# Kernel tuning notes

Hardware: AMD Instinct MI355X
Metric: run time of the kernel (lower is better)

The kernel has to match this reference:

```python
import jax, jax.numpy as jnp
import numpy as np

D = 1024      # feat_dim
H = 16        # n_heads
HD = D // H   # head_dim
G = 32        # number of image/text groups
P = 128       # patch tokens per image
T = 32        # text tokens per caption
SUM_P = G * P # 4096
BT = G * T    # 1024


def setup_inputs() -> dict:
    key = jax.random.key(0)
    ks = jax.random.split(key, 16)
    s = (6.0 / (2 * D)) ** 0.5  # xavier_uniform bound
    def xavier(k):
        return jax.random.uniform(k, (D, D), jnp.float32, -s, s)
    return {
        "V_token": jax.random.normal(ks[0], (SUM_P, D), jnp.float32),
        "L_token": jax.random.normal(ks[1], (BT, D), jnp.float32),
        "image_split_list": jnp.full((G,), P, dtype=jnp.int32),
        "text_split_list": jnp.full((G,), T, dtype=jnp.int32),
        "Wq_w": xavier(ks[2]), "Wq_b": jnp.zeros((D,), jnp.float32),
        "Wk_w": xavier(ks[3]), "Wk_b": jnp.zeros((D,), jnp.float32),
        "Wv_w": xavier(ks[4]), "Wv_b": jnp.zeros((D,), jnp.float32),
        "Wo_w": xavier(ks[5]), "Wo_b": jnp.zeros((D,), jnp.float32),
        "Wm_w": xavier(ks[6]), "Wm_b": jnp.zeros((D,), jnp.float32),
        "Wv2_w": xavier(ks[7]), "Wv2_b": jnp.zeros((D,), jnp.float32),
    }


def reference(V_token, L_token, image_split_list, text_split_list,
              Wq_w, Wq_b, Wk_w, Wk_b, Wv_w, Wv_b,
              Wo_w, Wo_b, Wm_w, Wm_b, Wv2_w, Wv2_b):
    sum_p, bt = V_token.shape[0], L_token.shape[0]
    g = image_split_list.shape[0]
    # segment ids (equivalent to torch.cat of torch.full per group)
    v_seg = jnp.repeat(jnp.arange(g), image_split_list, total_repeat_length=sum_p)
    l_seg = jnp.repeat(jnp.arange(g), text_split_list, total_repeat_length=bt)
    mask = v_seg[:, None] != l_seg[None, :]  # [sum_p, bt], True = masked out

    Q = (V_token @ Wq_w.T + Wq_b).reshape(sum_p, H, HD)
    K = (L_token @ Wk_w.T + Wk_b).reshape(bt, H, HD)
    Vl = (L_token @ Wv_w.T + Wv_b).reshape(bt, H, HD)

    scores = jnp.einsum('phd,thd->hpt', Q, K) / (HD ** 0.5)  # [H, sum_p, bt]
    scores = jnp.where(mask[None, :, :], -jnp.inf, scores)
    attn = jax.nn.softmax(scores, axis=-1)
    ctx = jnp.einsum('hpt,thd->phd', attn, Vl).reshape(sum_p, D)

    out = ctx @ Wo_w.T + Wo_b
    mu = out @ Wm_w.T + Wm_b
    log_var = out @ Wv2_w.T + Wv2_b
    return mu, log_var, attn
```

## Files before the change

### kernel.cpp

```cpp
#include <hip/hip_runtime.h>
#include <hip/hip_fp16.h>

typedef _Float16 f16x8 __attribute__((ext_vector_type(8)));
typedef _Float16 f16x4 __attribute__((ext_vector_type(4)));
typedef float f32x4_t __attribute__((ext_vector_type(4)));

struct CvtArgs {
  const float* src[8];
  _Float16* dst[8];
  int n4[8];
};

__global__ __launch_bounds__(256) void cvt_all(CvtArgs a) {
  const int t = blockIdx.y;
  const float4* __restrict__ in = (const float4*)a.src[t];
  f16x4* __restrict__ out = (f16x4*)a.dst[t];
  const int n4 = a.n4[t];
  const int stride = gridDim.x * blockDim.x;
  for (int i = blockIdx.x * blockDim.x + threadIdx.x; i < n4; i += stride) {
    float4 v = in[i];
    f16x4 h;
    h[0] = (_Float16)v.x; h[1] = (_Float16)v.y; h[2] = (_Float16)v.z; h[3] = (_Float16)v.w;
    out[i] = h;
  }
}

template <bool OUTH>
__device__ __forceinline__ void gemm_tile(const _Float16* __restrict__ A,
                                          const _Float16* __restrict__ W,
                                          const float* __restrict__ bias,
                                          void* __restrict__ Cv, int tm, int tn) {
  __shared__ _Float16 Ash[128][40];
  __shared__ _Float16 Bsh[64][40];

  const int tid = threadIdx.x;
  const int lane = tid & 63;
  const int wave = tid >> 6;
  const int wr = wave >> 1;
  const int wc = wave & 1;

  const int ar = tid >> 1;
  const int ac = (tid & 1) * 16;
  const int br = tid >> 2;
  const int bc = (tid & 3) * 8;

  const _Float16* Ag = A + (size_t)(tm + ar) * 1024 + ac;
  const _Float16* Bg = W + (size_t)(tn + br) * 1024 + bc;

  f32x4_t acc[4][2];
#pragma unroll
  for (int m = 0; m < 4; ++m)
#pragma unroll
    for (int n = 0; n < 2; ++n) acc[m][n] = (f32x4_t){0.f, 0.f, 0.f, 0.f};

  uint4 pa0 = *(const uint4*)(Ag);
  uint4 pa1 = *(const uint4*)(Ag + 8);
  uint4 pb = *(const uint4*)(Bg);

  const int fr = lane & 15;
  const int kc = (lane >> 4) * 8;

#pragma unroll 1
  for (int kt = 0; kt < 32; ++kt) {
    __syncthreads();
    *(uint4*)&Ash[ar][ac] = pa0;
    *(uint4*)&Ash[ar][ac + 8] = pa1;
    *(uint4*)&Bsh[br][bc] = pb;
    __syncthreads();
    if (kt + 1 < 32) {
      const int ko = (kt + 1) * 32;
      pa0 = *(const uint4*)(Ag + ko);
      pa1 = *(const uint4*)(Ag + ko + 8);
      pb = *(const uint4*)(Bg + ko);
    }
    f16x8 af[4], bf[2];
#pragma unroll
    for (int m = 0; m < 4; ++m) af[m] = *(const f16x8*)&Ash[wr * 64 + m * 16 + fr][kc];
#pragma unroll
    for (int n = 0; n < 2; ++n) bf[n] = *(const f16x8*)&Bsh[wc * 32 + n * 16 + fr][kc];
#pragma unroll
    for (int m = 0; m < 4; ++m)
#pragma unroll
      for (int n = 0; n < 2; ++n)
        acc[m][n] = __builtin_amdgcn_mfma_f32_16x16x32_f16(af[m], bf[n], acc[m][n], 0, 0, 0);
  }

  const int cr = (lane >> 4) * 4;
  const int cc = lane & 15;
#pragma unroll
  for (int m = 0; m < 4; ++m) {
#pragma unroll
    for (int n = 0; n < 2; ++n) {
      const int col = tn + wc * 32 + n * 16 + cc;
      const float bv = bias[col];
#pragma unroll
      for (int r = 0; r < 4; ++r) {
        const int row = tm + wr * 64 + m * 16 + cr + r;
        float v = acc[m][n][r] + bv;
        if (OUTH)
          ((_Float16*)Cv)[(size_t)row * 1024 + col] = (_Float16)v;
        else
          ((float*)Cv)[(size_t)row * 1024 + col] = v;
      }
    }
  }
}

__global__ __launch_bounds__(256) void gemm_qkv_fill(
    const _Float16* __restrict__ hV, const _Float16* __restrict__ hL,
    const _Float16* __restrict__ hWq, const _Float16* __restrict__ hWk,
    const _Float16* __restrict__ hWv,
    const float* __restrict__ bq, const float* __restrict__ bk, const float* __restrict__ bv,
    float* __restrict__ Qf, float* __restrict__ Kf, float* __restrict__ Vf,
    float* __restrict__ attn) {
  const int z = blockIdx.z;
  if (z == 3) {
    const int bl = blockIdx.y * 32 + blockIdx.x;
    float4* base = (float4*)attn + (size_t)bl * 16384;
    const float4 z4 = {0.f, 0.f, 0.f, 0.f};
#pragma unroll
    for (int c = threadIdx.x; c < 16384; c += 256) base[c] = z4;
    return;
  }
  if (z != 0 && blockIdx.x >= 8) return;

  const _Float16* A = (z == 0) ? hV : hL;
  const _Float16* W = (z == 0) ? hWq : (z == 1) ? hWk : hWv;
  const float* bias = (z == 0) ? bq : (z == 1) ? bk : bv;
  float* C = (z == 0) ? Qf : (z == 1) ? Kf : Vf;
  gemm_tile<false>(A, W, bias, (void*)C, blockIdx.x * 128, blockIdx.y * 64);
}

__global__ __launch_bounds__(256) void gemm_wo(
    const _Float16* __restrict__ ctx, const _Float16* __restrict__ hWo,
    const float* __restrict__ bo, _Float16* __restrict__ outh) {
  gemm_tile<true>(ctx, hWo, bo, (void*)outh, blockIdx.x * 128, blockIdx.y * 64);
}

__global__ __launch_bounds__(256) void gemm_mv_fill(
    const _Float16* __restrict__ outh,
    const _Float16* __restrict__ hWm, const _Float16* __restrict__ hWv2,
    const float* __restrict__ bm, const float* __restrict__ bv2,
    float* __restrict__ mu, float* __restrict__ logv, float* __restrict__ attn) {
  const int z = blockIdx.z;
  if (z == 2) {
    const int bl = blockIdx.y * 32 + blockIdx.x;
    const int wave = threadIdx.x >> 6;
    const int lane = threadIdx.x & 63;
    const float4 z4 = {0.f, 0.f, 0.f, 0.f};
#pragma unroll
    for (int i = 0; i < 16; ++i) {
      const int rowIdx = bl * 64 + i * 4 + wave;
      const int p = rowIdx & 4095;
      const int g8 = (p >> 7) * 8;
      float4* row = (float4*)(attn + ((size_t)(8 + (rowIdx >> 12)) * 4096 + p) * 1024);
#pragma unroll
      for (int c = lane; c < 256; c += 64) {
        if (c < g8 || c >= g8 + 8) row[c] = z4;
      }
    }
    return;
  }
  const _Float16* W = z ? hWv2 : hWm;
  const float* bias = z ? bv2 : bm;
  float* C = z ? logv : mu;
  gemm_tile<false>(outh, W, bias, (void*)C, blockIdx.x * 128, blockIdx.y * 64);
}

__global__ __launch_bounds__(256) void attn_kernel(
    const float* __restrict__ Q, const float* __restrict__ Kf, const float* __restrict__ Vf,
    float* __restrict__ attn_out,
    _Float16* __restrict__ ctx) {
  const int g = blockIdx.x;
  const int h = blockIdx.y;

  __shared__ float Ksh[32][68];
  __shared__ float Vsh[32][68];
  __shared__ float Arow[128][33];

  const int tid = threadIdx.x;

#pragma unroll
  for (int i = 0; i < 8; ++i) {
    int idx = tid + i * 256;
    int t = idx >> 6, d = idx & 63;
    Ksh[t][d] = Kf[(size_t)(g * 32 + t) * 1024 + h * 64 + d];
    Vsh[t][d] = Vf[(size_t)(g * 32 + t) * 1024 + h * 64 + d];
  }
  __syncthreads();

  const int p = tid >> 1;
  const int half = tid & 1;

  float4 qv[16];
  const float* qrow = Q + (size_t)(g * 128 + p) * 1024 + h * 64;
#pragma unroll
  for (int i = 0; i < 16; ++i) qv[i] = ((const float4*)qrow)[i];

  float s[16];
#pragma unroll
  for (int j = 0; j < 16; ++j) {
    int t = half * 16 + j;
    float acc = 0.f;
#pragma unroll
    for (int d4 = 0; d4 < 16; ++d4) {
      float4 kv = *(const float4*)&Ksh[t][d4 * 4];
      acc += qv[d4].x * kv.x + qv[d4].y * kv.y + qv[d4].z * kv.z + qv[d4].w * kv.w;
    }
    s[j] = acc * 0.125f;
  }

  float m = s[0];
#pragma unroll
  for (int j = 1; j < 16; ++j) m = fmaxf(m, s[j]);
  m = fmaxf(m, __shfl_xor(m, 1));
  float e[16];
  float sum = 0.f;
#pragma unroll
  for (int j = 0; j < 16; ++j) {
    e[j] = __expf(s[j] - m);
    sum += e[j];
  }
  sum += __shfl_xor(sum, 1);
  const float inv = 1.0f / sum;

  float* arow_out =
      attn_out + (size_t)h * 4096 * 1024 + (size_t)(g * 128 + p) * 1024 + g * 32 + half * 16;
#pragma unroll
  for (int j = 0; j < 16; ++j) {
    float a = e[j] * inv;
    arow_out[j] = a;
    Arow[p][half * 16 + j] = a;
  }
  __syncthreads();

  float4 acc4[8];
#pragma unroll
  for (int i = 0; i < 8; ++i) acc4[i] = (float4){0.f, 0.f, 0.f, 0.f};
#pragma unroll
  for (int t = 0; t < 32; ++t) {
    float av = Arow[p][t];
#pragma unroll
    for (int d4 = 0; d4 < 8; ++d4) {
      float4 v = *(const float4*)&Vsh[t][half * 32 + d4 * 4];
      acc4[d4].x += av * v.x;
      acc4[d4].y += av * v.y;
      acc4[d4].z += av * v.z;
      acc4[d4].w += av * v.w;
    }
  }
  _Float16* crow = ctx + (size_t)(g * 128 + p) * 1024 + h * 64 + half * 32;
#pragma unroll
  for (int i = 0; i < 4; ++i) {
    f16x8 hv;
    float4 lo = acc4[i * 2], hi = acc4[i * 2 + 1];
    hv[0] = (_Float16)lo.x; hv[1] = (_Float16)lo.y;
    hv[2] = (_Float16)lo.z; hv[3] = (_Float16)lo.w;
    hv[4] = (_Float16)hi.x; hv[5] = (_Float16)hi.y;
    hv[6] = (_Float16)hi.z; hv[7] = (_Float16)hi.w;
    *(f16x8*)&crow[i * 8] = hv;
  }
}

extern "C" void kernel_launch(void* const* d_in, const int* in_sizes, int n_in,
                              void* d_out, int out_size, void* d_ws, size_t ws_size,
                              hipStream_t stream) {
  const float* V_token = (const float*)d_in[0];
  const float* L_token = (const float*)d_in[1];
  const float* Wq_w = (const float*)d_in[4];
  const float* Wq_b = (const float*)d_in[5];
  const float* Wk_w = (const float*)d_in[6];
  const float* Wk_b = (const float*)d_in[7];
  const float* Wv_w = (const float*)d_in[8];
  const float* Wv_b = (const float*)d_in[9];
  const float* Wo_w = (const float*)d_in[10];
  const float* Wo_b = (const float*)d_in[11];
  const float* Wm_w = (const float*)d_in[12];
  const float* Wm_b = (const float*)d_in[13];
  const float* Wv2_w = (const float*)d_in[14];
  const float* Wv2_b = (const float*)d_in[15];

  char* ws = (char*)d_ws;
  _Float16* hV = (_Float16*)ws;   ws += (size_t)4096 * 1024 * 2;
  _Float16* hL = (_Float16*)ws;   ws += (size_t)1024 * 1024 * 2;
  _Float16* hWq = (_Float16*)ws;  ws += (size_t)1024 * 1024 * 2;
  _Float16* hWk = (_Float16*)ws;  ws += (size_t)1024 * 1024 * 2;
  _Float16* hWv = (_Float16*)ws;  ws += (size_t)1024 * 1024 * 2;
  _Float16* hWo = (_Float16*)ws;  ws += (size_t)1024 * 1024 * 2;
  _Float16* hWm = (_Float16*)ws;  ws += (size_t)1024 * 1024 * 2;
  _Float16* hWv2 = (_Float16*)ws; ws += (size_t)1024 * 1024 * 2;
  float* Qf = (float*)ws;         ws += (size_t)4096 * 1024 * 4;
  float* Kf = (float*)ws;         ws += (size_t)1024 * 1024 * 4;
  float* Vf = (float*)ws;         ws += (size_t)1024 * 1024 * 4;
  _Float16* ctx = (_Float16*)ws;  ws += (size_t)4096 * 1024 * 2;
  _Float16* outh = (_Float16*)ws; ws += (size_t)4096 * 1024 * 2;

  float* mu = (float*)d_out;
  float* logv = mu + (size_t)4096 * 1024;
  float* attn = mu + (size_t)2 * 4096 * 1024;

  CvtArgs ca;
  ca.src[0] = V_token; ca.dst[0] = hV;  ca.n4[0] = 4096 * 1024 / 4;
  ca.src[1] = L_token; ca.dst[1] = hL;  ca.n4[1] = 1024 * 1024 / 4;
  ca.src[2] = Wq_w;  ca.dst[2] = hWq;  ca.n4[2] = 1024 * 1024 / 4;
  ca.src[3] = Wk_w;  ca.dst[3] = hWk;  ca.n4[3] = 1024 * 1024 / 4;
  ca.src[4] = Wv_w;  ca.dst[4] = hWv;  ca.n4[4] = 1024 * 1024 / 4;
  ca.src[5] = Wo_w;  ca.dst[5] = hWo;  ca.n4[5] = 1024 * 1024 / 4;
  ca.src[6] = Wm_w;  ca.dst[6] = hWm;  ca.n4[6] = 1024 * 1024 / 4;
  ca.src[7] = Wv2_w; ca.dst[7] = hWv2; ca.n4[7] = 1024 * 1024 / 4;
  hipLaunchKernelGGL(cvt_all, dim3(128, 8), dim3(256), 0, stream, ca);

  hipLaunchKernelGGL(gemm_qkv_fill, dim3(32, 16, 4), dim3(256), 0, stream,
                     hV, hL, hWq, hWk, hWv, Wq_b, Wk_b, Wv_b, Qf, Kf, Vf, attn);

  hipLaunchKernelGGL(attn_kernel, dim3(32, 16), dim3(256), 0, stream, Qf, Kf, Vf, attn, ctx);

  hipLaunchKernelGGL(gemm_wo, dim3(32, 16), dim3(256), 0, stream, ctx, hWo, Wo_b, outh);

  hipLaunchKernelGGL(gemm_mv_fill, dim3(32, 16, 3), dim3(256), 0, stream,
                     outh, hWm, hWv2, Wm_b, Wv2_b, mu, logv, attn);
}
```

Measured before the change: 175.5 us.

## Double-buffer GEMM tiles with BK=64, store Q/K/V in fp16, flatten grids

The GEMM tile now uses double-buffered shared memory with a K-step of 64, which halves the barriers per K iteration and overlaps global prefetch with MFMA work. Q, K and V are written as fp16 instead of fp32, which cuts intermediate traffic; the attention kernel converts them back to float. The grids are flattened to 1D, which removes idle blocks for the K/V projections and gives the zero-fill blocks larger chunks. Q/K/V storage loses precision, and the larger shared tiles may reduce occupancy.

```diff
diff --git a/kernel.cpp b/kernel.cpp
--- a/kernel.cpp
+++ b/kernel.cpp
@@ -26,12 +26,12 @@
 }
 
 template <bool OUTH>
-__device__ __forceinline__ void gemm_tile(const _Float16* __restrict__ A,
-                                          const _Float16* __restrict__ W,
-                                          const float* __restrict__ bias,
-                                          void* __restrict__ Cv, int tm, int tn) {
-  __shared__ _Float16 Ash[128][40];
-  __shared__ _Float16 Bsh[64][40];
+__device__ __forceinline__ void gemm_tile64(const _Float16* __restrict__ A,
+                                            const _Float16* __restrict__ W,
+                                            const float* __restrict__ bias,
+                                            void* __restrict__ Cv, int tm, int tn) {
+  __shared__ _Float16 Ash[2][128][72];
+  __shared__ _Float16 Bsh[2][64][72];
 
   const int tid = threadIdx.x;
   const int lane = tid & 63;
@@ -39,13 +39,10 @@
   const int wr = wave >> 1;
   const int wc = wave & 1;
 
-  const int ar = tid >> 1;
-  const int ac = (tid & 1) * 16;
-  const int br = tid >> 2;
-  const int bc = (tid & 3) * 8;
-
-  const _Float16* Ag = A + (size_t)(tm + ar) * 1024 + ac;
-  const _Float16* Bg = W + (size_t)(tn + br) * 1024 + bc;
+  const int srow = tid >> 3;
+  const int scol = (tid & 7) * 8;
+  const _Float16* Ag = A + (size_t)(tm + srow) * 1024 + scol;
+  const _Float16* Bg = W + (size_t)(tn + srow) * 1024 + scol;
 
   f32x4_t acc[4][2];
 #pragma unroll
@@ -53,36 +50,61 @@
 #pragma unroll
     for (int n = 0; n < 2; ++n) acc[m][n] = (f32x4_t){0.f, 0.f, 0.f, 0.f};
 
-  uint4 pa0 = *(const uint4*)(Ag);
-  uint4 pa1 = *(const uint4*)(Ag + 8);
-  uint4 pb = *(const uint4*)(Bg);
+  uint4 ra[4], rb[2];
+
+#pragma unroll
+  for (int i = 0; i < 4; ++i) ra[i] = *(const uint4*)(Ag + (size_t)(i * 32) * 1024);
+#pragma unroll
+  for (int i = 0; i < 2; ++i) rb[i] = *(const uint4*)(Bg + (size_t)(i * 32) * 1024);
+#pragma unroll
+  for (int i = 0; i < 4; ++i) *(uint4*)&Ash[0][srow + i * 32][scol] = ra[i];
+#pragma unroll
+  for (int i = 0; i < 2; ++i) *(uint4*)&Bsh[0][srow + i * 32][scol] = rb[i];
+#pragma unroll
+  for (int i = 0; i < 4; ++i) ra[i] = *(const uint4*)(Ag + (size_t)(i * 32) * 1024 + 64);
+#pragma unroll
+  for (int i = 0; i < 2; ++i) rb[i] = *(const uint4*)(Bg + (size_t)(i * 32) * 1024 + 64);
+  __syncthreads();
 
   const int fr = lane & 15;
   const int kc = (lane >> 4) * 8;
 
 #pragma unroll 1
-  for (int kt = 0; kt < 32; ++kt) {
+  for (int t = 0; t < 16; ++t) {
+    const int cur = t & 1;
+    f16x8 af[2][4], bf[2][2];
+#pragma unroll
+    for (int ks = 0; ks < 2; ++ks) {
+#pragma unroll
+      for (int m = 0; m < 4; ++m)
+        af[ks][m] = *(const f16x8*)&Ash[cur][wr * 64 + m * 16 + fr][ks * 32 + kc];
+#pragma unroll
+      for (int n = 0; n < 2; ++n)
+        bf[ks][n] = *(const f16x8*)&Bsh[cur][wc * 32 + n * 16 + fr][ks * 32 + kc];
+    }
+#pragma unroll
+    for (int ks = 0; ks < 2; ++ks)
+#pragma unroll
+      for (int m = 0; m < 4; ++m)
+#pragma unroll
+        for (int n = 0; n < 2; ++n)
+          acc[m][n] =
+              __builtin_amdgcn_mfma_f32_16x16x32_f16(af[ks][m], bf[ks][n], acc[m][n], 0, 0, 0);
+    if (t < 15) {
+#pragma unroll
+      for (int i = 0; i < 4; ++i) *(uint4*)&Ash[cur ^ 1][srow + i * 32][scol] = ra[i];
+#pragma unroll
+      for (int i = 0; i < 2; ++i) *(uint4*)&Bsh[cur ^ 1][srow + i * 32][scol] = rb[i];
+    }
+    if (t < 14) {
+#pragma unroll
+      for (int i = 0; i < 4; ++i)
+        ra[i] = *(const uint4*)(Ag + (size_t)(i * 32) * 1024 + (t + 2) * 64);
+#pragma unroll
+      for (int i = 0; i < 2; ++i)
+        rb[i] = *(const uint4*)(Bg + (size_t)(i * 32) * 1024 + (t + 2) * 64);
+    }
     __syncthreads();
-    *(uint4*)&Ash[ar][ac] = pa0;
-    *(uint4*)&Ash[ar][ac + 8] = pa1;
-    *(uint4*)&Bsh[br][bc] = pb;
-    __syncthreads();
-    if (kt + 1 < 32) {
-      const int ko = (kt + 1) * 32;
-      pa0 = *(const uint4*)(Ag + ko);
-      pa1 = *(const uint4*)(Ag + ko + 8);
-      pb = *(const uint4*)(Bg + ko);
-    }
-    f16x8 af[4], bf[2];
-#pragma unroll
-    for (int m = 0; m < 4; ++m) af[m] = *(const f16x8*)&Ash[wr * 64 + m * 16 + fr][kc];
-#pragma unroll
-    for (int n = 0; n < 2; ++n) bf[n] = *(const f16x8*)&Bsh[wc * 32 + n * 16 + fr][kc];
-#pragma unroll
-    for (int m = 0; m < 4; ++m)
-#pragma unroll
-      for (int n = 0; n < 2; ++n)
-        acc[m][n] = __builtin_amdgcn_mfma_f32_16x16x32_f16(af[m], bf[n], acc[m][n], 0, 0, 0);
   }
 
   const int cr = (lane >> 4) * 4;
@@ -111,30 +133,34 @@
     const _Float16* __restrict__ hWq, const _Float16* __restrict__ hWk,
     const _Float16* __restrict__ hWv,
     const float* __restrict__ bq, const float* __restrict__ bk, const float* __restrict__ bv,
-    float* __restrict__ Qf, float* __restrict__ Kf, float* __restrict__ Vf,
+    _Float16* __restrict__ Qh, _Float16* __restrict__ Kh, _Float16* __restrict__ Vh,
     float* __restrict__ attn) {
-  const int z = blockIdx.z;
-  if (z == 3) {
-    const int bl = blockIdx.y * 32 + blockIdx.x;
-    float4* base = (float4*)attn + (size_t)bl * 16384;
+  int b = blockIdx.x;
+  if (b < 256) {
+    float4* base = (float4*)attn + (size_t)b * 32768;
     const float4 z4 = {0.f, 0.f, 0.f, 0.f};
-#pragma unroll
-    for (int c = threadIdx.x; c < 16384; c += 256) base[c] = z4;
-    return;
-  }
-  if (z != 0 && blockIdx.x >= 8) return;
-
-  const _Float16* A = (z == 0) ? hV : hL;
-  const _Float16* W = (z == 0) ? hWq : (z == 1) ? hWk : hWv;
-  const float* bias = (z == 0) ? bq : (z == 1) ? bk : bv;
-  float* C = (z == 0) ? Qf : (z == 1) ? Kf : Vf;
-  gemm_tile<false>(A, W, bias, (void*)C, blockIdx.x * 128, blockIdx.y * 64);
+    for (int i = threadIdx.x; i < 32768; i += 256) base[i] = z4;
+    return;
+  }
+  b -= 256;
+  if (b < 512) {
+    gemm_tile64<true>(hV, hWq, bq, (void*)Qh, (b >> 4) * 128, (b & 15) * 64);
+    return;
+  }
+  b -= 512;
+  if (b < 128) {
+    gemm_tile64<true>(hL, hWk, bk, (void*)Kh, (b >> 4) * 128, (b & 15) * 64);
+    return;
+  }
+  b -= 128;
+  gemm_tile64<true>(hL, hWv, bv, (void*)Vh, (b >> 4) * 128, (b & 15) * 64);
 }
 
 __global__ __launch_bounds__(256) void gemm_wo(
     const _Float16* __restrict__ ctx, const _Float16* __restrict__ hWo,
     const float* __restrict__ bo, _Float16* __restrict__ outh) {
-  gemm_tile<true>(ctx, hWo, bo, (void*)outh, blockIdx.x * 128, blockIdx.y * 64);
+  const int b = blockIdx.x;
+  gemm_tile64<true>(ctx, hWo, bo, (void*)outh, (b >> 4) * 128, (b & 15) * 64);
 }
 
 __global__ __launch_bounds__(256) void gemm_mv_fill(
@@ -142,33 +168,33 @@
     const _Float16* __restrict__ hWm, const _Float16* __restrict__ hWv2,
     const float* __restrict__ bm, const float* __restrict__ bv2,
     float* __restrict__ mu, float* __restrict__ logv, float* __restrict__ attn) {
-  const int z = blockIdx.z;
-  if (z == 2) {
-    const int bl = blockIdx.y * 32 + blockIdx.x;
+  int b = blockIdx.x;
+  if (b < 256) {
     const int wave = threadIdx.x >> 6;
     const int lane = threadIdx.x & 63;
     const float4 z4 = {0.f, 0.f, 0.f, 0.f};
-#pragma unroll
-    for (int i = 0; i < 16; ++i) {
-      const int rowIdx = bl * 64 + i * 4 + wave;
+    for (int i = 0; i < 32; ++i) {
+      const int rowIdx = b * 128 + i * 4 + wave;
       const int p = rowIdx & 4095;
       const int g8 = (p >> 7) * 8;
       float4* row = (float4*)(attn + ((size_t)(8 + (rowIdx >> 12)) * 4096 + p) * 1024);
-#pragma unroll
-      for (int c = lane; c < 256; c += 64) {
+      for (int c = lane; c < 256; c += 64)
         if (c < g8 || c >= g8 + 8) row[c] = z4;
-      }
-    }
-    return;
-  }
-  const _Float16* W = z ? hWv2 : hWm;
-  const float* bias = z ? bv2 : bm;
-  float* C = z ? logv : mu;
-  gemm_tile<false>(outh, W, bias, (void*)C, blockIdx.x * 128, blockIdx.y * 64);
+    }
+    return;
+  }
+  b -= 256;
+  if (b < 512) {
+    gemm_tile64<false>(outh, hWm, bm, (void*)mu, (b >> 4) * 128, (b & 15) * 64);
+    return;
+  }
+  b -= 512;
+  gemm_tile64<false>(outh, hWv2, bv2, (void*)logv, (b >> 4) * 128, (b & 15) * 64);
 }
 
 __global__ __launch_bounds__(256) void attn_kernel(
-    const float* __restrict__ Q, const float* __restrict__ Kf, const float* __restrict__ Vf,
+    const _Float16* __restrict__ Qh, const _Float16* __restrict__ Kh,
+    const _Float16* __restrict__ Vh,
     float* __restrict__ attn_out,
     _Float16* __restrict__ ctx) {
   const int g = blockIdx.x;
@@ -179,34 +205,37 @@
   __shared__ float Arow[128][33];
 
   const int tid = threadIdx.x;
-
-#pragma unroll
-  for (int i = 0; i < 8; ++i) {
-    int idx = tid + i * 256;
-    int t = idx >> 6, d = idx & 63;
-    Ksh[t][d] = Kf[(size_t)(g * 32 + t) * 1024 + h * 64 + d];
-    Vsh[t][d] = Vf[(size_t)(g * 32 + t) * 1024 + h * 64 + d];
+  {
+    const int r = tid >> 3, c8 = (tid & 7) * 8;
+    f16x8 kv = *(const f16x8*)(Kh + (size_t)(g * 32 + r) * 1024 + h * 64 + c8);
+    f16x8 vv = *(const f16x8*)(Vh + (size_t)(g * 32 + r) * 1024 + h * 64 + c8);
+#pragma unroll
+    for (int j = 0; j < 8; ++j) {
+      Ksh[r][c8 + j] = (float)kv[j];
+      Vsh[r][c8 + j] = (float)vv[j];
+    }
   }
   __syncthreads();
 
   const int p = tid >> 1;
   const int half = tid & 1;
 
-  float4 qv[16];
-  const float* qrow = Q + (size_t)(g * 128 + p) * 1024 + h * 64;
-#pragma unroll
-  for (int i = 0; i < 16; ++i) qv[i] = ((const float4*)qrow)[i];
+  float qf[64];
+  const f16x8* qp = (const f16x8*)(Qh + (size_t)(g * 128 + p) * 1024 + h * 64);
+#pragma unroll
+  for (int i = 0; i < 8; ++i) {
+    f16x8 v = qp[i];
+#pragma unroll
+    for (int j = 0; j < 8; ++j) qf[i * 8 + j] = (float)v[j];
+  }
 
   float s[16];
 #pragma unroll
   for (int j = 0; j < 16; ++j) {
-    int t = half * 16 + j;
+    const int t = half * 16 + j;
     float acc = 0.f;
 #pragma unroll
-    for (int d4 = 0; d4 < 16; ++d4) {
-      float4 kv = *(const float4*)&Ksh[t][d4 * 4];
-      acc += qv[d4].x * kv.x + qv[d4].y * kv.y + qv[d4].z * kv.z + qv[d4].w * kv.w;
-    }
+    for (int d = 0; d < 64; ++d) acc += qf[d] * Ksh[t][d];
     s[j] = acc * 0.125f;
   }
 
@@ -239,7 +268,7 @@
   for (int i = 0; i < 8; ++i) acc4[i] = (float4){0.f, 0.f, 0.f, 0.f};
 #pragma unroll
   for (int t = 0; t < 32; ++t) {
-    float av = Arow[p][t];
+    const float av = Arow[p][t];
 #pragma unroll
     for (int d4 = 0; d4 < 8; ++d4) {
       float4 v = *(const float4*)&Vsh[t][half * 32 + d4 * 4];
@@ -289,9 +318,9 @@
   _Float16* hWo = (_Float16*)ws;  ws += (size_t)1024 * 1024 * 2;
   _Float16* hWm = (_Float16*)ws;  ws += (size_t)1024 * 1024 * 2;
   _Float16* hWv2 = (_Float16*)ws; ws += (size_t)1024 * 1024 * 2;
-  float* Qf = (float*)ws;         ws += (size_t)4096 * 1024 * 4;
-  float* Kf = (float*)ws;         ws += (size_t)1024 * 1024 * 4;
-  float* Vf = (float*)ws;         ws += (size_t)1024 * 1024 * 4;
+  _Float16* Qh = (_Float16*)ws;   ws += (size_t)4096 * 1024 * 2;
+  _Float16* Kh = (_Float16*)ws;   ws += (size_t)1024 * 1024 * 2;
+  _Float16* Vh = (_Float16*)ws;   ws += (size_t)1024 * 1024 * 2;
   _Float16* ctx = (_Float16*)ws;  ws += (size_t)4096 * 1024 * 2;
   _Float16* outh = (_Float16*)ws; ws += (size_t)4096 * 1024 * 2;
 
@@ -310,13 +339,13 @@
   ca.src[7] = Wv2_w; ca.dst[7] = hWv2; ca.n4[7] = 1024 * 1024 / 4;
   hipLaunchKernelGGL(cvt_all, dim3(128, 8), dim3(256), 0, stream, ca);
 
-  hipLaunchKernelGGL(gemm_qkv_fill, dim3(32, 16, 4), dim3(256), 0, stream,
-                     hV, hL, hWq, hWk, hWv, Wq_b, Wk_b, Wv_b, Qf, Kf, Vf, attn);
-
-  hipLaunchKernelGGL(attn_kernel, dim3(32, 16), dim3(256), 0, stream, Qf, Kf, Vf, attn, ctx);
-
-  hipLaunchKernelGGL(gemm_wo, dim3(32, 16), dim3(256), 0, stream, ctx, hWo, Wo_b, outh);
-
-  hipLaunchKernelGGL(gemm_mv_fill, dim3(32, 16, 3), dim3(256), 0, stream,
+  hipLaunchKernelGGL(gemm_qkv_fill, dim3(1024), dim3(256), 0, stream,
+                     hV, hL, hWq, hWk, hWv, Wq_b, Wk_b, Wv_b, Qh, Kh, Vh, attn);
+
+  hipLaunchKernelGGL(attn_kernel, dim3(32, 16), dim3(256), 0, stream, Qh, Kh, Vh, attn, ctx);
+
+  hipLaunchKernelGGL(gemm_wo, dim3(512), dim3(256), 0, stream, ctx, hWo, Wo_b, outh);
+
+  hipLaunchKernelGGL(gemm_mv_fill, dim3(1280), dim3(256), 0, stream,
                      outh, hWm, hWv2, Wm_b, Wv2_b, mu, logv, attn);
 }
```

Result: slower. 280.6 us (+59.8%).
